# Performance work log

Hardware: AMD Instinct MI355X
Metric: run time of the kernel (lower is better)

## Reference

```python
import jax, jax.numpy as jnp
import numpy as np

TAU = 2.0
EPS_G = 1e-10   # gumbel numerical eps
EPS_H = 1e-12   # entropy log eps


def _gumbel(u):
    # u ~ Uniform(0,1) -> standard Gumbel noise
    return -jnp.log(-jnp.log(u + EPS_G) + EPS_G)


def setup_inputs() -> dict:
    key = jax.random.key(0)
    k1, k2, k3, k4 = jax.random.split(key, 4)
    B, T, D, K = 4, 1024, 512, 8192
    x = jax.random.normal(k1, (B, T, D), dtype=jnp.float32)
    codebook = jax.random.normal(k2, (K, D), dtype=jnp.float32)
    u1 = jax.random.uniform(k3, (B * T, K), dtype=jnp.float32)
    u2 = jax.random.uniform(k4, (B * T, K), dtype=jnp.float32)
    return {"x": x, "codebook": codebook, "u1": u1, "u2": u2}


def reference(x, codebook, u1, u2):
    B, T, D = x.shape
    x_flat = x.reshape(-1, D)                                  # (N, D)
    x_sq = jnp.sum(x_flat * x_flat, axis=1, keepdims=True)     # (N, 1)
    c_sq = jnp.sum(codebook * codebook, axis=1)                # (K,)
    xc = x_flat @ codebook.T                                   # (N, K)
    logits = -(x_sq + c_sq - 2.0 * xc)                         # -||x - c||^2

    # soft gumbel-softmax (first independent noise draw)
    probs_soft = jax.nn.softmax((logits + _gumbel(u1)) / TAU, axis=-1)  # (N, K)
    quantized_soft = (probs_soft @ codebook).reshape(B, T, D)

    # hard gumbel-softmax indices (second independent noise draw);
    # argmax of the hard one-hot == argmax of perturbed logits
    indices = jnp.argmax(logits + _gumbel(u2), axis=-1).reshape(B, T)

    codebook_loss = jnp.mean((quantized_soft - jax.lax.stop_gradient(x)) ** 2)
    enc_commitment_loss = jnp.mean((x - jax.lax.stop_gradient(quantized_soft)) ** 2)

    entropy = -jnp.sum(probs_soft * jnp.log(probs_soft + EPS_H), axis=1)  # (N,)
    mean_entropy = jnp.mean(entropy)

    return quantized_soft, indices, codebook_loss, enc_commitment_loss, mean_entropy
```

## Files before the change

kernel.cpp:

```cpp
#include <hip/hip_runtime.h>
#include <math.h>

#define NROWS 4096
#define KCODES 8192
#define DDIM 512
#define IDX_OFF 2097152
#define L0_OFF  2101248
#define L1_OFF  2101249
#define ENT_OFF 2101250
#define ARGMAX_MARGIN 0.05f
#define FIX_CHUNK 256
#define FIX_CPR (KCODES / FIX_CHUNK)

#define TOP2_UPD(v1, k1, v2, k2, h, k)                                 \
    do {                                                               \
        if ((h) > (v1)) { v2 = v1; k2 = k1; v1 = (h); k1 = (k); }      \
        else if ((h) > (v2)) { v2 = (h); k2 = (k); }                   \
    } while (0)

typedef __attribute__((ext_vector_type(8))) short bf16x8;
typedef __attribute__((ext_vector_type(4))) float f32x4;

__device__ __forceinline__ float gumbelfast(float u) {
    float a = __logf(u + 1e-10f);
    float b = __logf(1e-10f - a);
    return -b;
}
__device__ __forceinline__ ushort f2bf(float f) {
    uint u = __float_as_uint(f);
    return (ushort)((u + 0x7FFFu + ((u >> 16) & 1u)) >> 16);
}
__device__ __forceinline__ float bf2f(ushort h) {
    return __uint_as_float(((uint)h) << 16);
}

__device__ __forceinline__ float np_log32(float x) {
    return (float)log((double)x);
}
__device__ __forceinline__ float np_gumbel(float u) {
    float a  = __fadd_rn(u, 1e-10f);
    float la = np_log32(a);
    float b  = __fadd_rn(-la, 1e-10f);
    float lb = np_log32(b);
    return -lb;
}
__device__ float np_sumsq512(const float* __restrict__ a) {
    float blk[4];
    #pragma unroll
    for (int b = 0; b < 4; ++b) {
        const float* p = a + b * 128;
        float r[8];
        #pragma unroll
        for (int j = 0; j < 8; ++j) r[j] = __fmul_rn(p[j], p[j]);
        for (int i = 8; i < 128; i += 8) {
            #pragma unroll
            for (int j = 0; j < 8; ++j)
                r[j] = __fadd_rn(r[j], __fmul_rn(p[i + j], p[i + j]));
        }
        blk[b] = __fadd_rn(__fadd_rn(__fadd_rn(r[0], r[1]), __fadd_rn(r[2], r[3])),
                           __fadd_rn(__fadd_rn(r[4], r[5]), __fadd_rn(r[6], r[7])));
    }
    return __fadd_rn(__fadd_rn(blk[0], blk[1]), __fadd_rn(blk[2], blk[3]));
}

__device__ __forceinline__ float dot4(float4 a, float4 b) {
    return a.x*b.x + a.y*b.y + a.z*b.z + a.w*b.w;
}
__device__ __forceinline__ void fma4(float4& o, float p, float4 c) {
    o.x += p*c.x; o.y += p*c.y; o.z += p*c.z; o.w += p*c.w;
}

__global__ __launch_bounds__(256) void vq_csq2(const float* __restrict__ cb,
                                               float* __restrict__ csq,
                                               int* __restrict__ flag_cnt) {
    if (blockIdx.x == 0 && threadIdx.x == 0) flag_cnt[0] = 0;
    const int tid = threadIdx.x;
    const int row = blockIdx.x * 8 + (tid >> 5);
    const int rl  = tid & 31;
    const int b   = rl >> 3, j = rl & 7;
    const float* p = cb + (size_t)row * DDIM + b * 128 + j;
    float r = __fmul_rn(p[0], p[0]);
    #pragma unroll
    for (int i = 1; i < 16; ++i) {
        float v = p[i * 8];
        r = __fadd_rn(r, __fmul_rn(v, v));
    }
    r = __fadd_rn(r, __shfl_xor(r, 1));
    r = __fadd_rn(r, __shfl_xor(r, 2));
    r = __fadd_rn(r, __shfl_xor(r, 4));
    r = __fadd_rn(r, __shfl_xor(r, 8));
    r = __fadd_rn(r, __shfl_xor(r, 16));
    if (rl == 0) csq[row] = r;
}

__global__ __launch_bounds__(256) void vq_fixup(
        const float* __restrict__ x, const float* __restrict__ cb,
        const float* __restrict__ u2, const float* __restrict__ csq,
        const int* __restrict__ flag_cnt, const int* __restrict__ flag_rows,
        float* __restrict__ out) {
    __shared__ float xrow[DDIM];
    __shared__ float bv[4];
    __shared__ int   bk[4];
    const int n = flag_cnt[0];
    for (int w = blockIdx.x; w < n; w += gridDim.x) {
        const int row = flag_rows[w];
        for (int i = threadIdx.x; i < DDIM; i += 256)
            xrow[i] = x[(size_t)row * DDIM + i];
        __syncthreads();
        const float xsq = np_sumsq512(xrow);
        float best = -1e30f; int bidx = 0x7fffffff;
        for (int k = threadIdx.x; k < KCODES; k += 256) {
            const float* c = cb + (size_t)k * DDIM;
            float acc1 = 0.f, acc2 = 0.f;
            #pragma unroll 8
            for (int d = 0; d < 384; ++d) acc1 = fmaf(xrow[d], c[d], acc1);
            #pragma unroll 8
            for (int d = 384; d < DDIM; ++d) acc2 = fmaf(xrow[d], c[d], acc2);
            float xc = __fadd_rn(acc1, acc2);
            float t1 = __fadd_rn(xsq, csq[k]);
            float t2 = __fmul_rn(2.0f, xc);
            float t3 = __fsub_rn(t1, t2);
            float logit = -t3;
            float h = __fadd_rn(logit, np_gumbel(u2[(size_t)row * KCODES + k]));
            if (h > best || (h == best && k < bidx)) { best = h; bidx = k; }
        }
        const int lane = threadIdx.x & 63, wv = threadIdx.x >> 6;
        #pragma unroll
        for (int m = 32; m >= 1; m >>= 1) {
            float ov = __shfl_xor(best, m); int ok = __shfl_xor(bidx, m);
            if (ov > best || (ov == best && ok < bidx)) { best = ov; bidx = ok; }
        }
        if (lane == 0) { bv[wv] = best; bk[wv] = bidx; }
        __syncthreads();
        if (threadIdx.x == 0) {
            float b = bv[0]; int bi = bk[0];
            #pragma unroll
            for (int i = 1; i < 4; ++i)
                if (bv[i] > b || (bv[i] == b && bk[i] < bi)) { b = bv[i]; bi = bk[i]; }
            out[IDX_OFF + row] = (float)bi;
        }
        __syncthreads();
    }
}

__global__ __launch_bounds__(256) void vq_fixup2(
        const float* __restrict__ x, const float* __restrict__ cb,
        const float* __restrict__ u2, const float* __restrict__ csq,
        const int* __restrict__ flag_cnt, const int* __restrict__ flag_rows,
        unsigned long long* __restrict__ packed) {
    __shared__ float xrow[DDIM];
    __shared__ float xsq_sh;
    __shared__ unsigned long long redp[4];
    const int n = flag_cnt[0];
    const int total = n * FIX_CPR;
    for (int item = blockIdx.x; item < total; item += gridDim.x) {
        const int w = item / FIX_CPR;
        const int chunk = item - w * FIX_CPR;
        const int row = flag_rows[w];
        __syncthreads();
        for (int i = threadIdx.x; i < DDIM; i += 256)
            xrow[i] = x[(size_t)row * DDIM + i];
        __syncthreads();
        if (threadIdx.x == 0) xsq_sh = np_sumsq512(xrow);
        __syncthreads();
        const float xsq = xsq_sh;
        const int k = chunk * FIX_CHUNK + threadIdx.x;
        const float* c = cb + (size_t)k * DDIM;
        float acc1 = 0.f, acc2 = 0.f;
        #pragma unroll 8
        for (int d = 0; d < 384; ++d) acc1 = fmaf(xrow[d], c[d], acc1);
        #pragma unroll 8
        for (int d = 384; d < DDIM; ++d) acc2 = fmaf(xrow[d], c[d], acc2);
        float xc = __fadd_rn(acc1, acc2);
        float t1 = __fadd_rn(xsq, csq[k]);
        float t2 = __fmul_rn(2.0f, xc);
        float logit = -__fsub_rn(t1, t2);
        float h = __fadd_rn(logit, np_gumbel(u2[(size_t)row * KCODES + k]));
        uint hb = __float_as_uint(h);
        uint key = (hb & 0x80000000u) ? ~hb : (hb | 0x80000000u);
        unsigned long long val = ((unsigned long long)key << 32)
                               | (unsigned long long)(0xFFFFFFFFu - (uint)k);
        #pragma unroll
        for (int m = 32; m >= 1; m >>= 1) {
            unsigned long long o = __shfl_xor(val, m);
            if (o > val) val = o;
        }
        if ((threadIdx.x & 63) == 0) redp[threadIdx.x >> 6] = val;
        __syncthreads();
        if (threadIdx.x == 0) {
            unsigned long long v = redp[0];
            if (redp[1] > v) v = redp[1];
            if (redp[2] > v) v = redp[2];
            if (redp[3] > v) v = redp[3];
            atomicMax(&packed[row], v);
        }
    }
}


__global__ __launch_bounds__(256) void vq_split(const float4* __restrict__ in,
                                                ushort* __restrict__ hi,
                                                ushort* __restrict__ lo) {
    int i = blockIdx.x * 256 + threadIdx.x;
    float4 v = in[i];
    ushort4 h, l;
    h.x = f2bf(v.x); h.y = f2bf(v.y); h.z = f2bf(v.z); h.w = f2bf(v.w);
    l.x = f2bf(v.x - bf2f(h.x)); l.y = f2bf(v.y - bf2f(h.y));
    l.z = f2bf(v.z - bf2f(h.z)); l.w = f2bf(v.w - bf2f(h.w));
    ((ushort4*)hi)[i] = h;
    ((ushort4*)lo)[i] = l;
}

__global__ __launch_bounds__(256) void vq_prep_cb(const float* __restrict__ cb,
                                                  ushort* __restrict__ chi,
                                                  ushort* __restrict__ clo,
                                                  ushort* __restrict__ cbT) {
    __shared__ ushort T[64][65];
    const int k0 = blockIdx.x * 64, d0 = blockIdx.y * 64;
    const int lane = threadIdx.x & 63, w = threadIdx.x >> 6;
    #pragma unroll
    for (int i = 0; i < 16; ++i) {
        int ky = i * 4 + w;
        size_t g = (size_t)(k0 + ky) * DDIM + d0 + lane;
        float f = cb[g];
        ushort h = f2bf(f);
        chi[g] = h;
        clo[g] = f2bf(f - bf2f(h));
        T[lane][ky] = h;
    }
    __syncthreads();
    #pragma unroll
    for (int i = 0; i < 16; ++i) {
        int dy = i * 4 + w;
        cbT[(size_t)(d0 + dy) * KCODES + k0 + lane] = T[dy][lane];
    }
}

__global__ __launch_bounds__(256) void vq_gemm1(
        const ushort* __restrict__ xhi, const ushort* __restrict__ xlo,
        const ushort* __restrict__ chi, const ushort* __restrict__ clo,
        const float* __restrict__ csq, float* __restrict__ S0) {
    __shared__ short As[2][128 * 72];
    __shared__ short Bs[2][128 * 72];
    const int tid = threadIdx.x;
    const int lane = tid & 63, wid = tid >> 6;
    const int wr = wid >> 1, wc = wid & 1;
    const int m0 = blockIdx.y * 128, n0 = blockIdx.x * 128;

    bf16x8 sAh[4], sAl[4], sBh[4], sBl[4];
    f32x4 acc[4][4] = {};

    #define G1_LOAD(kkv)                                                       \
        do {                                                                   \
            const int k0_ = (kkv) * 64;                                        \
            _Pragma("unroll")                                                  \
            for (int i = 0; i < 4; ++i) {                                      \
                int c = tid + i * 256;                                         \
                int row = c >> 3, off = (c & 7) * 8;                           \
                size_t gA = (size_t)(m0 + row) * DDIM + k0_ + off;             \
                size_t gB = (size_t)(n0 + row) * DDIM + k0_ + off;             \
                sAh[i] = *(const bf16x8*)(xhi + gA);                           \
                sAl[i] = *(const bf16x8*)(xlo + gA);                           \
                sBh[i] = *(const bf16x8*)(chi + gB);                           \
                sBl[i] = *(const bf16x8*)(clo + gB);                           \
            }                                                                  \
        } while (0)

    #define G1_WRITE()                                                         \
        do {                                                                   \
            _Pragma("unroll")                                                  \
            for (int i = 0; i < 4; ++i) {                                      \
                int c = tid + i * 256;                                         \
                int row = c >> 3, off = (c & 7) * 8;                           \
                int lidx = row * 72 + off;                                     \
                *(bf16x8*)&As[0][lidx] = sAh[i];                               \
                *(bf16x8*)&As[1][lidx] = sAl[i];                               \
                *(bf16x8*)&Bs[0][lidx] = sBh[i];                               \
                *(bf16x8*)&Bs[1][lidx] = sBl[i];                               \
            }                                                                  \
        } while (0)

    G1_LOAD(0);
    G1_WRITE();
    __syncthreads();
    for (int kk = 0; kk < 8; ++kk) {
        if (kk < 7) G1_LOAD(kk + 1);
        #pragma unroll
        for (int ks = 0; ks < 2; ++ks) {
            const int ko = ks * 32 + (lane >> 4) * 8;
            bf16x8 ah[4], al[4], bh[4], bl[4];
            #pragma unroll
            for (int m = 0; m < 4; ++m) {
                int r = wr * 64 + m * 16 + (lane & 15);
                ah[m] = *(bf16x8*)&As[0][r * 72 + ko];
                al[m] = *(bf16x8*)&As[1][r * 72 + ko];
            }
            #pragma unroll
            for (int n = 0; n < 4; ++n) {
                int r = wc * 64 + n * 16 + (lane & 15);
                bh[n] = *(bf16x8*)&Bs[0][r * 72 + ko];
                bl[n] = *(bf16x8*)&Bs[1][r * 72 + ko];
            }
            #pragma unroll
            for (int m = 0; m < 4; ++m)
                #pragma unroll
                for (int n = 0; n < 4; ++n) {
                    acc[m][n] = __builtin_amdgcn_mfma_f32_16x16x32_bf16(ah[m], bh[n], acc[m][n], 0, 0, 0);
                    acc[m][n] = __builtin_amdgcn_mfma_f32_16x16x32_bf16(ah[m], bl[n], acc[m][n], 0, 0, 0);
                    acc[m][n] = __builtin_amdgcn_mfma_f32_16x16x32_bf16(al[m], bh[n], acc[m][n], 0, 0, 0);
                }
        }
        if (kk < 7) {
            __syncthreads();
            G1_WRITE();
            __syncthreads();
        }
    }
    #undef G1_LOAD
    #undef G1_WRITE

    #pragma unroll
    for (int n = 0; n < 4; ++n) {
        int col = n0 + wc * 64 + n * 16 + (lane & 15);
        float cq = csq[col];
        #pragma unroll
        for (int m = 0; m < 4; ++m) {
            int rbase = m0 + wr * 64 + m * 16 + ((lane >> 4) << 2);
            #pragma unroll
            for (int j = 0; j < 4; ++j)
                S0[(size_t)(rbase + j) * KCODES + col] = 2.0f * acc[m][n][j] - cq;
        }
    }
}

__global__ __launch_bounds__(1024) void vq_soft(
        float* __restrict__ S0, const float* __restrict__ u1,
        const float* __restrict__ u2,
        float* __restrict__ Aarr, float* __restrict__ entarr,
        float* __restrict__ out, int* __restrict__ flag_cnt,
        int* __restrict__ flag_rows, unsigned long long* __restrict__ packed) {
    __shared__ float redm[16], redA[16], redB[16];
    __shared__ float rv1[16], rv2[16];
    __shared__ int   rk1[16], rk2[16];
    const int row = blockIdx.x, tid = threadIdx.x;
    const int lane = tid & 63, wid = tid >> 6;
    const size_t base = (size_t)row * KCODES;
    if (tid == 0) packed[row] = 0ULL;

    const int ka = tid * 4;
    const int kb = 4096 + tid * 4;
    float4 Sa = *(const float4*)(S0 + base + ka);
    float4 Sb = *(const float4*)(S0 + base + kb);
    float4 Ua = *(const float4*)(u1 + base + ka);
    float4 Ub = *(const float4*)(u1 + base + kb);
    float4 Va = *(const float4*)(u2 + base + ka);
    float4 Vb = *(const float4*)(u2 + base + kb);

    float v1 = -1e30f, v2 = -1e30f; int k1 = 0x7fffffff, k2 = 0x7fffffff;
    float h;
    h = Sa.x + gumbelfast(Va.x); TOP2_UPD(v1, k1, v2, k2, h, ka);
    h = Sa.y + gumbelfast(Va.y); TOP2_UPD(v1, k1, v2, k2, h, ka + 1);
    h = Sa.z + gumbelfast(Va.z); TOP2_UPD(v1, k1, v2, k2, h, ka + 2);
    h = Sa.w + gumbelfast(Va.w); TOP2_UPD(v1, k1, v2, k2, h, ka + 3);
    h = Sb.x + gumbelfast(Vb.x); TOP2_UPD(v1, k1, v2, k2, h, kb);
    h = Sb.y + gumbelfast(Vb.y); TOP2_UPD(v1, k1, v2, k2, h, kb + 1);
    h = Sb.z + gumbelfast(Vb.z); TOP2_UPD(v1, k1, v2, k2, h, kb + 2);
    h = Sb.w + gumbelfast(Vb.w); TOP2_UPD(v1, k1, v2, k2, h, kb + 3);

    float4 sa, sb;
    sa.x = (Sa.x + gumbelfast(Ua.x)) * 0.5f;
    sa.y = (Sa.y + gumbelfast(Ua.y)) * 0.5f;
    sa.z = (Sa.z + gumbelfast(Ua.z)) * 0.5f;
    sa.w = (Sa.w + gumbelfast(Ua.w)) * 0.5f;
    sb.x = (Sb.x + gumbelfast(Ub.x)) * 0.5f;
    sb.y = (Sb.y + gumbelfast(Ub.y)) * 0.5f;
    sb.z = (Sb.z + gumbelfast(Ub.z)) * 0.5f;
    sb.w = (Sb.w + gumbelfast(Ub.w)) * 0.5f;
    float mloc = fmaxf(fmaxf(fmaxf(sa.x, sa.y), fmaxf(sa.z, sa.w)),
                       fmaxf(fmaxf(sb.x, sb.y), fmaxf(sb.z, sb.w)));
    #pragma unroll
    for (int m = 32; m >= 1; m >>= 1) mloc = fmaxf(mloc, __shfl_xor(mloc, m));
    if (lane == 0) redm[wid] = mloc;
    __syncthreads();
    float mrow = redm[0];
    #pragma unroll
    for (int i = 1; i < 16; ++i) mrow = fmaxf(mrow, redm[i]);

    float A, Be;
    {
        float d0 = sa.x - mrow, d1 = sa.y - mrow, d2 = sa.z - mrow, d3 = sa.w - mrow;
        float e0 = __expf(d0), e1 = __expf(d1), e2 = __expf(d2), e3 = __expf(d3);
        float d4 = sb.x - mrow, d5 = sb.y - mrow, d6 = sb.z - mrow, d7 = sb.w - mrow;
        float e4 = __expf(d4), e5 = __expf(d5), e6 = __expf(d6), e7 = __expf(d7);
        A  = (((e0 + e1) + e2) + e3) + ((((e4 + e5) + e6) + e7));
        Be = (((e0*d0 + e1*d1) + e2*d2) + e3*d3) + ((((e4*d4 + e5*d5) + e6*d6) + e7*d7));
        ushort* Prow = (ushort*)(S0 + base);
        ushort4 pa, pb;
        pa.x = f2bf(e0); pa.y = f2bf(e1); pa.z = f2bf(e2); pa.w = f2bf(e3);
        pb.x = f2bf(e4); pb.y = f2bf(e5); pb.z = f2bf(e6); pb.w = f2bf(e7);
        *(ushort4*)(Prow + ka) = pa;
        *(ushort4*)(Prow + kb) = pb;
    }
    #pragma unroll
    for (int m = 32; m >= 1; m >>= 1) { A += __shfl_xor(A, m); Be += __shfl_xor(Be, m); }
    #pragma unroll
    for (int m = 32; m >= 1; m >>= 1) {
        float ov1 = __shfl_xor(v1, m); int ok1 = __shfl_xor(k1, m);
        float ov2 = __shfl_xor(v2, m); int ok2 = __shfl_xor(k2, m);
        if (ov1 > v1 || (ov1 == v1 && ok1 < k1)) {
            float nv2; int nk2;
            if (v1 > ov2 || (v1 == ov2 && k1 < ok2)) { nv2 = v1; nk2 = k1; }
            else { nv2 = ov2; nk2 = ok2; }
            v1 = ov1; k1 = ok1; v2 = nv2; k2 = nk2;
        } else if (ov1 > v2 || (ov1 == v2 && ok1 < k2)) { v2 = ov1; k2 = ok1; }
    }
    if (lane == 0) {
        redA[wid] = A; redB[wid] = Be;
        rv1[wid] = v1; rv2[wid] = v2; rk1[wid] = k1; rk2[wid] = k2;
    }
    __syncthreads();
    if (tid == 0) {
        float At = 0.f, Bt = 0.f;
        #pragma unroll
        for (int i = 0; i < 16; ++i) { At += redA[i]; Bt += redB[i]; }
        float V1 = rv1[0], V2 = rv2[0]; int K1 = rk1[0], K2 = rk2[0];
        #pragma unroll
        for (int i = 1; i < 16; ++i) {
            float ov1 = rv1[i], ov2 = rv2[i]; int ok1 = rk1[i], ok2 = rk2[i];
            if (ov1 > V1 || (ov1 == V1 && ok1 < K1)) {
                float nv2; int nk2;
                if (V1 > ov2 || (V1 == ov2 && K1 < ok2)) { nv2 = V1; nk2 = K1; }
                else { nv2 = ov2; nk2 = ok2; }
                V1 = ov1; K1 = ok1; V2 = nv2; K2 = nk2;
            } else if (ov1 > V2 || (ov1 == V2 && ok1 < K2)) { V2 = ov1; K2 = ok1; }
        }
        Aarr[row] = At;
        entarr[row] = logf(At) - Bt / At;
        out[IDX_OFF + row] = (float)K1;
        if (V1 - V2 < ARGMAX_MARGIN) {
            int s = atomicAdd(flag_cnt, 1);
            flag_rows[s] = row;
        }
    }
}

#define G2_BK 128
__global__ __launch_bounds__(512) void vq_gemm2b(
        const ushort* __restrict__ P, const ushort* __restrict__ cbT,
        const float* __restrict__ Aarr, const float* __restrict__ x,
        float* __restrict__ out, float* __restrict__ wloss) {
    __shared__ short Ap[2][128 * 136];
    __shared__ short Bt[2][64 * 136];
    __shared__ float redl[8];
    const int tid = threadIdx.x;
    const int lane = tid & 63, wid = tid >> 6;
    const int wr = wid & 3, wc = wid >> 2;
    const int bid = blockIdx.x;
    const int mblk = bid & 31, nblk = bid >> 5;
    const int m0 = mblk * 128, n0 = nblk * 64;

    bf16x8 rp[4], rb[2];
    f32x4 acc[2][2] = {};

    #define G2_LOAD(t)                                                         \
        do {                                                                   \
            const int k0_ = (t) * G2_BK;                                       \
            _Pragma("unroll")                                                  \
            for (int i = 0; i < 4; ++i) {                                      \
                int c = tid + i * 512;                                         \
                int row = c >> 4, off = (c & 15) * 8;                          \
                rp[i] = *(const bf16x8*)(P + (size_t)(m0 + row) * 16384 + k0_ + off); \
            }                                                                  \
            _Pragma("unroll")                                                  \
            for (int i = 0; i < 2; ++i) {                                      \
                int c = tid + i * 512;                                         \
                int row = c >> 4, off = (c & 15) * 8;                          \
                rb[i] = *(const bf16x8*)(cbT + (size_t)(n0 + row) * 8192 + k0_ + off); \
            }                                                                  \
        } while (0)

    #define G2_WRITE(buf)                                                      \
        do {                                                                   \
            _Pragma("unroll")                                                  \
            for (int i = 0; i < 4; ++i) {                                      \
                int c = tid + i * 512;                                         \
                int row = c >> 4, off = (c & 15) * 8;                          \
                *(bf16x8*)&Ap[buf][row * 136 + off] = rp[i];                   \
            }                                                                  \
            _Pragma("unroll")                                                  \
            for (int i = 0; i < 2; ++i) {                                      \
                int c = tid + i * 512;                                         \
                int row = c >> 4, off = (c & 15) * 8;                          \
                *(bf16x8*)&Bt[buf][row * 136 + off] = rb[i];                   \
            }                                                                  \
        } while (0)

    G2_LOAD(0);
    G2_WRITE(0);
    __syncthreads();
    int cur = 0;
    for (int t = 0; t < KCODES / G2_BK; ++t) {
        if (t < KCODES / G2_BK - 1) G2_LOAD(t + 1);
        #pragma unroll
        for (int ks = 0; ks < 4; ++ks) {
            const int ko = ks * 32 + (lane >> 4) * 8;
            bf16x8 af[2], bfr[2];
            #pragma unroll
            for (int m = 0; m < 2; ++m)
                af[m] = *(bf16x8*)&Ap[cur][(wr * 32 + m * 16 + (lane & 15)) * 136 + ko];
            #pragma unroll
            for (int n = 0; n < 2; ++n)
                bfr[n] = *(bf16x8*)&Bt[cur][(wc * 32 + n * 16 + (lane & 15)) * 136 + ko];
            #pragma unroll
            for (int m = 0; m < 2; ++m)
                #pragma unroll
                for (int n = 0; n < 2; ++n)
                    acc[m][n] = __builtin_amdgcn_mfma_f32_16x16x32_bf16(af[m], bfr[n], acc[m][n], 0, 0, 0);
        }
        if (t < KCODES / G2_BK - 1) {
            __syncthreads();
            G2_WRITE(cur ^ 1);
            __syncthreads();
            cur ^= 1;
        }
    }
    #undef G2_LOAD
    #undef G2_WRITE

    float lsum = 0.f;
    #pragma unroll
    for (int n = 0; n < 2; ++n) {
        int col = n0 + wc * 32 + n * 16 + (lane & 15);
        #pragma unroll
        for (int m = 0; m < 2; ++m) {
            int rbase = m0 + wr * 32 + m * 16 + ((lane >> 4) << 2);
            #pragma unroll
            for (int j = 0; j < 4; ++j) {
                int row = rbase + j;
                float inva = 1.0f / Aarr[row];
                float q = acc[m][n][j] * inva;
                out[(size_t)row * DDIM + col] = q;
                float d = q - x[(size_t)row * DDIM + col];
                lsum += d * d;
            }
        }
    }
    #pragma unroll
    for (int m = 32; m >= 1; m >>= 1) lsum += __shfl_xor(lsum, m);
    if (lane == 0) redl[wid] = lsum;
    __syncthreads();
    if (tid == 0) {
        float s = 0.f;
        #pragma unroll
        for (int i = 0; i < 8; ++i) s += redl[i];
        wloss[bid] = s;
    }
}

__global__ __launch_bounds__(256) void vq_finalize2(
        const float* __restrict__ wloss, const float* __restrict__ entarr,
        const int* __restrict__ flag_cnt, const int* __restrict__ flag_rows,
        const unsigned long long* __restrict__ packed, float* __restrict__ out) {
    __shared__ float redl[4], rede[4];
    int tid = threadIdx.x;
    const int n = flag_cnt[0];
    for (int w = tid; w < n; w += 256) {
        int row = flag_rows[w];
        uint lowbits = (uint)(packed[row] & 0xFFFFFFFFULL);
        out[IDX_OFF + row] = (float)(0xFFFFFFFFu - lowbits);
    }
    float l = wloss[tid];
    float e = 0.f;
    #pragma unroll
    for (int i = 0; i < 16; ++i) e += entarr[tid + i * 256];
    #pragma unroll
    for (int m = 32; m >= 1; m >>= 1) { l += __shfl_xor(l, m); e += __shfl_xor(e, m); }
    if ((tid & 63) == 0) { redl[tid >> 6] = l; rede[tid >> 6] = e; }
    __syncthreads();
    if (tid == 0) {
        float L = (((redl[0] + redl[1]) + redl[2]) + redl[3]) * (1.0f / 2097152.0f);
        float E = (((rede[0] + rede[1]) + rede[2]) + rede[3]) * (1.0f / 4096.0f);
        out[L0_OFF]  = L;
        out[L1_OFF]  = L;
        out[ENT_OFF] = E;
    }
}

#define BR 16
#define KT 128
#define NUM_KT 64
#define NUM_DC 4

__device__ __forceinline__ float gumbelf(float u) {
    return -logf(-logf(u + 1e-10f) + 1e-10f);
}

__global__ __launch_bounds__(256) void vq_main_fb(
        const float* __restrict__ x, const float* __restrict__ cb,
        const float* __restrict__ u1, const float* __restrict__ u2,
        const float* __restrict__ csq, float* __restrict__ out,
        float* __restrict__ wloss, float* __restrict__ went,
        int* __restrict__ flag_cnt, int* __restrict__ flag_rows) {
    __shared__ float4 Xs[BR][129];
    __shared__ float4 Cs[KT * 32];
    __shared__ float4 Ol[BR][128];
    __shared__ float4 Ps[BR][32];
    __shared__ float  xsq_s[BR];
    __shared__ float  f_s[BR];
    __shared__ float  A_s[BR];
    __shared__ float  ent_s[BR];
    __shared__ float  red4[4];

    const int tid = threadIdx.x;
    const int rg  = tid >> 5;
    const int cg  = tid & 31;
    const int r0  = rg * 2;
    const int r1  = r0 + 1;
    const int row0g = blockIdx.x * BR;
    const float4* cb4 = (const float4*)cb;

    {
        const float4* xg = (const float4*)x + (size_t)row0g * 128;
        #pragma unroll
        for (int i = 0; i < 8; ++i) {
            int idx = tid + i * 256;
            int r = idx >> 7, q = idx & 127;
            Xs[r][q] = xg[r * 128 + q];
            Ol[r][q] = make_float4(0.f, 0.f, 0.f, 0.f);
        }
    }
    __syncthreads();
    {
        int r = tid >> 4, part = tid & 15;
        float s = 0.f;
        #pragma unroll
        for (int q = 0; q < 8; ++q) {
            float4 v = Xs[r][part * 8 + q];
            s += v.x*v.x + v.y*v.y + v.z*v.z + v.w*v.w;
        }
        #pragma unroll
        for (int m = 8; m >= 1; m >>= 1) s += __shfl_xor(s, m);
        if (part == 0) xsq_s[r] = s;
    }
    __syncthreads();
    const float xsq0 = xsq_s[r0];
    const float xsq1 = xsq_s[r1];

    float m0 = -1e30f, m1 = -1e30f;
    float A0 = 0.f, A1 = 0.f;
    float B0 = 0.f, B1 = 0.f;
    float hb0 = -1e30f, hb1 = -1e30f;
    float hc0 = -1e30f, hc1 = -1e30f;
    int   kb0 = 0, kb1 = 0, kc0 = 0, kc1 = 0;

    for (int t = 0; t < NUM_KT; ++t) {
        const int ktb = t * KT;
        float a00=0.f,a01=0.f,a02=0.f,a03=0.f,a10=0.f,a11=0.f,a12=0.f,a13=0.f;

        for (int dc = 0; dc < NUM_DC; ++dc) {
            #pragma unroll
            for (int i = 0; i < 16; ++i) {
                int idx = tid + i * 256;
                int k = idx >> 5, q = idx & 31;
                Cs[k * 32 + (q ^ ((k >> 2) & 7))] =
                    cb4[(size_t)(ktb + k) * 128 + dc * 32 + q];
            }
            __syncthreads();
            const int qb = dc * 32;
            const int c4 = cg * 4;
            #pragma unroll 4
            for (int dd = 0; dd < 32; ++dd) {
                float4 xv0 = Xs[r0][qb + dd];
                float4 xv1 = Xs[r1][qb + dd];
                int swq = dd ^ (cg & 7);
                float4 cv0 = Cs[(c4 + 0) * 32 + swq];
                float4 cv1 = Cs[(c4 + 1) * 32 + swq];
                float4 cv2 = Cs[(c4 + 2) * 32 + swq];
                float4 cv3 = Cs[(c4 + 3) * 32 + swq];
                a00 += dot4(xv0, cv0); a01 += dot4(xv0, cv1);
                a02 += dot4(xv0, cv2); a03 += dot4(xv0, cv3);
                a10 += dot4(xv1, cv0); a11 += dot4(xv1, cv1);
                a12 += dot4(xv1, cv2); a13 += dot4(xv1, cv3);
            }
            __syncthreads();
        }
        {
            const int kg0 = ktb + cg * 4;
            size_t ur0 = (size_t)(row0g + r0) * KCODES + kg0;
            size_t ur1 = (size_t)(row0g + r1) * KCODES + kg0;
            float4 u1a = *(const float4*)(u1 + ur0);
            float4 u1b = *(const float4*)(u1 + ur1);
            float4 u2a = *(const float4*)(u2 + ur0);
            float4 u2b = *(const float4*)(u2 + ur1);
            float cs0 = csq[kg0], cs1 = csq[kg0+1], cs2 = csq[kg0+2], cs3 = csq[kg0+3];
            {
                float l0 = 2.f*a00 - xsq0 - cs0;
                float l1 = 2.f*a01 - xsq0 - cs1;
                float l2 = 2.f*a02 - xsq0 - cs2;
                float l3 = 2.f*a03 - xsq0 - cs3;
                float h;
                h = l0 + gumbelf(u2a.x); TOP2_UPD(hb0, kb0, hc0, kc0, h, kg0);
                h = l1 + gumbelf(u2a.y); TOP2_UPD(hb0, kb0, hc0, kc0, h, kg0+1);
                h = l2 + gumbelf(u2a.z); TOP2_UPD(hb0, kb0, hc0, kc0, h, kg0+2);
                h = l3 + gumbelf(u2a.w); TOP2_UPD(hb0, kb0, hc0, kc0, h, kg0+3);
                float s0 = (l0 + gumbelf(u1a.x)) * 0.5f;
                float s1 = (l1 + gumbelf(u1a.y)) * 0.5f;
                float s2 = (l2 + gumbelf(u1a.z)) * 0.5f;
                float s3 = (l3 + gumbelf(u1a.w)) * 0.5f;
                float tmax = fmaxf(fmaxf(s0, s1), fmaxf(s2, s3));
                #pragma unroll
                for (int m = 16; m >= 1; m >>= 1) tmax = fmaxf(tmax, __shfl_xor(tmax, m));
                float mn = fmaxf(m0, tmax);
                float p0 = expf(s0 - mn), p1 = expf(s1 - mn);
                float p2 = expf(s2 - mn), p3 = expf(s3 - mn);
                float tA = p0 + p1 + p2 + p3;
                float tB = p0*(s0-mn) + p1*(s1-mn) + p2*(s2-mn) + p3*(s3-mn);
                #pragma unroll
                for (int m = 16; m >= 1; m >>= 1) { tA += __shfl_xor(tA, m); tB += __shfl_xor(tB, m); }
                float f = expf(m0 - mn);
                B0 = f * (B0 + (m0 - mn) * A0) + tB;
                A0 = f * A0 + tA;
                m0 = mn;
                Ps[r0][cg] = make_float4(p0, p1, p2, p3);
                if (cg == 0) f_s[r0] = f;
            }
            {
                float l0 = 2.f*a10 - xsq1 - cs0;
                float l1 = 2.f*a11 - xsq1 - cs1;
                float l2 = 2.f*a12 - xsq1 - cs2;
                float l3 = 2.f*a13 - xsq1 - cs3;
                float h;
                h = l0 + gumbelf(u2b.x); TOP2_UPD(hb1, kb1, hc1, kc1, h, kg0);
                h = l1 + gumbelf(u2b.y); TOP2_UPD(hb1, kb1, hc1, kc1, h, kg0+1);
                h = l2 + gumbelf(u2b.z); TOP2_UPD(hb1, kb1, hc1, kc1, h, kg0+2);
                h = l3 + gumbelf(u2b.w); TOP2_UPD(hb1, kb1, hc1, kc1, h, kg0+3);
                float s0 = (l0 + gumbelf(u1b.x)) * 0.5f;
                float s1 = (l1 + gumbelf(u1b.y)) * 0.5f;
                float s2 = (l2 + gumbelf(u1b.z)) * 0.5f;
                float s3 = (l3 + gumbelf(u1b.w)) * 0.5f;
                float tmax = fmaxf(fmaxf(s0, s1), fmaxf(s2, s3));
                #pragma unroll
                for (int m = 16; m >= 1; m >>= 1) tmax = fmaxf(tmax, __shfl_xor(tmax, m));
                float mn = fmaxf(m1, tmax);
                float p0 = expf(s0 - mn), p1 = expf(s1 - mn);
                float p2 = expf(s2 - mn), p3 = expf(s3 - mn);
                float tA = p0 + p1 + p2 + p3;
                float tB = p0*(s0-mn) + p1*(s1-mn) + p2*(s2-mn) + p3*(s3-mn);
                #pragma unroll
                for (int m = 16; m >= 1; m >>= 1) { tA += __shfl_xor(tA, m); tB += __shfl_xor(tB, m); }
                float f = expf(m1 - mn);
                B1 = f * (B1 + (m1 - mn) * A1) + tB;
                A1 = f * A1 + tA;
                m1 = mn;
                Ps[r1][cg] = make_float4(p0, p1, p2, p3);
                if (cg == 0) f_s[r1] = f;
            }
        }
        __syncthreads();

        for (int dc = 0; dc < NUM_DC; ++dc) {
            #pragma unroll
            for (int i = 0; i < 16; ++i) {
                int idx = tid + i * 256;
                int k = idx >> 5, q = idx & 31;
                Cs[k * 32 + (q ^ ((k >> 2) & 7))] =
                    cb4[(size_t)(ktb + k) * 128 + dc * 32 + q];
            }
            __syncthreads();
            float4 o0 = make_float4(0.f,0.f,0.f,0.f);
            float4 o1 = make_float4(0.f,0.f,0.f,0.f);
            #pragma unroll 2
            for (int k4 = 0; k4 < 32; ++k4) {
                float4 pv0 = Ps[r0][k4];
                float4 pv1 = Ps[r1][k4];
                int sq = cg ^ (k4 & 7);
                float4 cva = Cs[(k4*4 + 0) * 32 + sq];
                float4 cvb = Cs[(k4*4 + 1) * 32 + sq];
                float4 cvc = Cs[(k4*4 + 2) * 32 + sq];
                float4 cvd = Cs[(k4*4 + 3) * 32 + sq];
                fma4(o0, pv0.x, cva); fma4(o0, pv0.y, cvb);
                fma4(o0, pv0.z, cvc); fma4(o0, pv0.w, cvd);
                fma4(o1, pv1.x, cva); fma4(o1, pv1.y, cvb);
                fma4(o1, pv1.z, cvc); fma4(o1, pv1.w, cvd);
            }
            float fr0 = f_s[r0], fr1 = f_s[r1];
            int oq = dc * 32 + cg;
            float4 Ov0 = Ol[r0][oq];
            Ov0.x = Ov0.x*fr0 + o0.x; Ov0.y = Ov0.y*fr0 + o0.y;
            Ov0.z = Ov0.z*fr0 + o0.z; Ov0.w = Ov0.w*fr0 + o0.w;
            Ol[r0][oq] = Ov0;
            float4 Ov1 = Ol[r1][oq];
            Ov1.x = Ov1.x*fr1 + o1.x; Ov1.y = Ov1.y*fr1 + o1.y;
            Ov1.z = Ov1.z*fr1 + o1.z; Ov1.w = Ov1.w*fr1 + o1.w;
            Ol[r1][oq] = Ov1;
            __syncthreads();
        }
    }
    {
        float ent0 = logf(A0) - B0 / A0;
        float v1 = hb0, v2 = hc0; int k1 = kb0, k2 = kc0;
        #pragma unroll
        for (int m = 16; m >= 1; m >>= 1) {
            float ov1 = __shfl_xor(v1, m); int ok1 = __shfl_xor(k1, m);
            float ov2 = __shfl_xor(v2, m); int ok2 = __shfl_xor(k2, m);
            if (ov1 > v1 || (ov1 == v1 && ok1 < k1)) {
                float nv2; int nk2;
                if (v1 > ov2 || (v1 == ov2 && k1 < ok2)) { nv2 = v1; nk2 = k1; }
                else { nv2 = ov2; nk2 = ok2; }
                v1 = ov1; k1 = ok1; v2 = nv2; k2 = nk2;
            } else if (ov1 > v2 || (ov1 == v2 && ok1 < k2)) {
                v2 = ov1; k2 = ok1;
            }
        }
        if (cg == 0) {
            out[IDX_OFF + row0g + r0] = (float)k1;
            if (v1 - v2 < ARGMAX_MARGIN) {
                int s = atomicAdd(flag_cnt, 1);
                flag_rows[s] = row0g + r0;
            }
            ent_s[r0] = ent0;
            A_s[r0] = A0;
        }
        float ent1 = logf(A1) - B1 / A1;
        v1 = hb1; v2 = hc1; k1 = kb1; k2 = kc1;
        #pragma unroll
        for (int m = 16; m >= 1; m >>= 1) {
            float ov1 = __shfl_xor(v1, m); int ok1 = __shfl_xor(k1, m);
            float ov2 = __shfl_xor(v2, m); int ok2 = __shfl_xor(k2, m);
            if (ov1 > v1 || (ov1 == v1 && ok1 < k1)) {
                float nv2; int nk2;
                if (v1 > ov2 || (v1 == ov2 && k1 < ok2)) { nv2 = v1; nk2 = k1; }
                else { nv2 = ov2; nk2 = ok2; }
                v1 = ov1; k1 = ok1; v2 = nv2; k2 = nk2;
            } else if (ov1 > v2 || (ov1 == v2 && ok1 < k2)) {
                v2 = ov1; k2 = ok1;
            }
        }
        if (cg == 0) {
            out[IDX_OFF + row0g + r1] = (float)k1;
            if (v1 - v2 < ARGMAX_MARGIN) {
                int s = atomicAdd(flag_cnt, 1);
                flag_rows[s] = row0g + r1;
            }
            ent_s[r1] = ent1;
            A_s[r1] = A1;
        }
    }
    __syncthreads();

    float lsum = 0.f;
    float4* outq = (float4*)out;
    #pragma unroll
    for (int i = 0; i < 8; ++i) {
        int idx = tid + i * 256;
        int r = idx >> 7, q = idx & 127;
        float inva = 1.f / A_s[r];
        float4 Ov = Ol[r][q];
        float4 qv = make_float4(Ov.x*inva, Ov.y*inva, Ov.z*inva, Ov.w*inva);
        outq[(size_t)(row0g + r) * 128 + q] = qv;
        float4 xv = Xs[r][q];
        float dx;
        dx = qv.x - xv.x; lsum += dx*dx;
        dx = qv.y - xv.y; lsum += dx*dx;
        dx = qv.z - xv.z; lsum += dx*dx;
        dx = qv.w - xv.w; lsum += dx*dx;
    }
    #pragma unroll
    for (int m = 32; m >= 1; m >>= 1) lsum += __shfl_xor(lsum, m);
    if ((tid & 63) == 0) red4[tid >> 6] = lsum;
    __syncthreads();
    if (tid == 0) {
        wloss[blockIdx.x] = red4[0] + red4[1] + red4[2] + red4[3];
        float es = 0.f;
        for (int r = 0; r < BR; ++r) es += ent_s[r];
        went[blockIdx.x] = es;
    }
}

__global__ __launch_bounds__(256) void vq_finalize_fb(const float* __restrict__ wloss,
                                                      const float* __restrict__ went,
                                                      float* __restrict__ out) {
    __shared__ float redl[4], rede[4];
    int tid = threadIdx.x;
    float l = wloss[tid];
    float e = went[tid];
    #pragma unroll
    for (int m = 32; m >= 1; m >>= 1) { l += __shfl_xor(l, m); e += __shfl_xor(e, m); }
    if ((tid & 63) == 0) { redl[tid >> 6] = l; rede[tid >> 6] = e; }
    __syncthreads();
    if (tid == 0) {
        float L = (redl[0] + redl[1] + redl[2] + redl[3]) * (1.0f / 2097152.0f);
        float E = (rede[0] + rede[1] + rede[2] + rede[3]) * (1.0f / 4096.0f);
        out[L0_OFF]  = L;
        out[L1_OFF]  = L;
        out[ENT_OFF] = E;
    }
}

extern "C" void kernel_launch(void* const* d_in, const int* in_sizes, int n_in,
                              void* d_out, int out_size, void* d_ws, size_t ws_size,
                              hipStream_t stream) {
    const float* x  = (const float*)d_in[0];
    const float* cb = (const float*)d_in[1];
    const float* u1 = (const float*)d_in[2];
    const float* u2 = (const float*)d_in[3];
    float* out = (float*)d_out;

    const size_t NEED = 0xA018000ULL;
    if (ws_size >= NEED) {
        char* w = (char*)d_ws;
        float*  S0   = (float*)w;
        ushort* xhi  = (ushort*)(w + 0x8000000);
        ushort* xlo  = (ushort*)(w + 0x8400000);
        ushort* chi  = (ushort*)(w + 0x8800000);
        ushort* clo  = (ushort*)(w + 0x9000000);
        ushort* cbT  = (ushort*)(w + 0x9800000);
        float*  csq  = (float*)(w + 0xA000000);
        float*  Aarr = (float*)(w + 0xA008000);
        float*  enta = (float*)(w + 0xA00C000);
        float*  wlp  = (float*)(w + 0xA010000);
        int*    fcnt = (int*)(w + 0xA010400);
        int*    frws = (int*)(w + 0xA010800);
        unsigned long long* packed = (unsigned long long*)(w + 0x8000000);

        vq_csq2<<<KCODES / 8, 256, 0, stream>>>(cb, csq, fcnt);
        vq_split<<<2048, 256, 0, stream>>>((const float4*)x, xhi, xlo);
        vq_prep_cb<<<dim3(128, 8), 256, 0, stream>>>(cb, chi, clo, cbT);
        vq_gemm1<<<dim3(64, 32), 256, 0, stream>>>(xhi, xlo, chi, clo, csq, S0);
        vq_soft<<<NROWS, 1024, 0, stream>>>(S0, u1, u2, Aarr, enta, out, fcnt, frws, packed);
        vq_gemm2b<<<256, 512, 0, stream>>>((const ushort*)S0, cbT, Aarr, x, out, wlp);
        vq_fixup2<<<1024, 256, 0, stream>>>(x, cb, u2, csq, fcnt, frws, packed);
        vq_finalize2<<<1, 256, 0, stream>>>(wlp, enta, fcnt, frws, packed, out);
    } else {
        float* ws  = (float*)d_ws;
        float* csq    = ws;
        float* wlossp = ws + KCODES;
        float* wentp  = ws + KCODES + 256;
        int*   fcnt   = (int*)(ws + KCODES + 512);
        int*   frows  = fcnt + 1;

        vq_csq2<<<KCODES / 8, 256, 0, stream>>>(cb, csq, fcnt);
        vq_main_fb<<<NROWS / BR, 256, 0, stream>>>(x, cb, u1, u2, csq, out,
                                                   wlossp, wentp, fcnt, frows);
        vq_fixup<<<256, 256, 0, stream>>>(x, cb, u2, csq, fcnt, frows, out);
        vq_finalize_fb<<<1, 256, 0, stream>>>(wlossp, wentp, out);
    }
}
```

Baseline: 367.5 us.

## Fuse hard-gumbel top-2 argmax into GEMM1 epilogue with packed sortable keys

```diff
diff --git a/kernel.cpp b/kernel.cpp
--- a/kernel.cpp
+++ b/kernel.cpp
@@ -32,6 +32,12 @@
 }
 __device__ __forceinline__ float bf2f(ushort h) {
     return __uint_as_float(((uint)h) << 16);
+}
+__device__ __forceinline__ unsigned long long hkey(float h, int k) {
+    uint hb = __float_as_uint(h);
+    uint kk = (hb & 0x80000000u) ? ~hb : (hb | 0x80000000u);
+    return ((unsigned long long)kk << 32)
+         | (unsigned long long)(0xFFFFFFFFu - (uint)k);
 }
 
 __device__ __forceinline__ float np_log32(float x) {
@@ -239,9 +245,11 @@
 __global__ __launch_bounds__(256) void vq_gemm1(
         const ushort* __restrict__ xhi, const ushort* __restrict__ xlo,
         const ushort* __restrict__ chi, const ushort* __restrict__ clo,
-        const float* __restrict__ csq, float* __restrict__ S0) {
+        const float* __restrict__ csq, const float* __restrict__ u2,
+        float* __restrict__ S0, ulonglong2* __restrict__ Htop) {
     __shared__ short As[2][128 * 72];
     __shared__ short Bs[2][128 * 72];
+    __shared__ ulonglong2 Top2L[128][2];
     const int tid = threadIdx.x;
     const int lane = tid & 63, wid = tid >> 6;
     const int wr = wid >> 1, wc = wid & 1;
@@ -319,29 +327,65 @@
     #undef G1_LOAD
     #undef G1_WRITE
 
+    const int colbase = n0 + wc * 64 + (lane & 15);
+    float cqv[4];
+    #pragma unroll
+    for (int n = 0; n < 4; ++n) cqv[n] = csq[colbase + n * 16];
+
     #pragma unroll
     for (int n = 0; n < 4; ++n) {
-        int col = n0 + wc * 64 + n * 16 + (lane & 15);
-        float cq = csq[col];
+        int col = colbase + n * 16;
         #pragma unroll
         for (int m = 0; m < 4; ++m) {
             int rbase = m0 + wr * 64 + m * 16 + ((lane >> 4) << 2);
             #pragma unroll
             for (int j = 0; j < 4; ++j)
-                S0[(size_t)(rbase + j) * KCODES + col] = 2.0f * acc[m][n][j] - cq;
-        }
+                S0[(size_t)(rbase + j) * KCODES + col] = 2.0f * acc[m][n][j] - cqv[n];
+        }
+    }
+
+    #pragma unroll
+    for (int m = 0; m < 4; ++m) {
+        #pragma unroll
+        for (int j = 0; j < 4; ++j) {
+            const int rl = wr * 64 + m * 16 + ((lane >> 4) << 2) + j;
+            const size_t ur = (size_t)(m0 + rl) * KCODES + colbase;
+            unsigned long long t1 = 0ULL, t2 = 0ULL;
+            #pragma unroll
+            for (int n = 0; n < 4; ++n) {
+                float S = 2.0f * acc[m][n][j] - cqv[n];
+                float h = S + gumbelfast(u2[ur + n * 16]);
+                unsigned long long key = hkey(h, colbase + n * 16);
+                if (key > t1) { t2 = t1; t1 = key; }
+                else if (key > t2) { t2 = key; }
+            }
+            #pragma unroll
+            for (int mm = 1; mm <= 8; mm <<= 1) {
+                unsigned long long b1 = __shfl_xor(t1, mm);
+                unsigned long long b2 = __shfl_xor(t2, mm);
+                if (b1 > t1) { unsigned long long t = t1; t1 = b1; t2 = (t > b2) ? t : b2; }
+                else         { t2 = (b1 > t2) ? b1 : t2; }
+            }
+            if ((lane & 15) == 0) Top2L[rl][wc] = make_ulonglong2(t1, t2);
+        }
+    }
+    __syncthreads();
+    if (tid < 128) {
+        ulonglong2 a = Top2L[tid][0], b = Top2L[tid][1];
+        unsigned long long r1, r2;
+        if (b.x > a.x) { r1 = b.x; r2 = (a.x > b.y) ? a.x : b.y; }
+        else           { r1 = a.x; r2 = (b.x > a.y) ? b.x : a.y; }
+        Htop[(size_t)(m0 + tid) * 64 + blockIdx.x] = make_ulonglong2(r1, r2);
     }
 }
 
 __global__ __launch_bounds__(1024) void vq_soft(
         float* __restrict__ S0, const float* __restrict__ u1,
-        const float* __restrict__ u2,
+        const ulonglong2* __restrict__ Htop,
         float* __restrict__ Aarr, float* __restrict__ entarr,
         float* __restrict__ out, int* __restrict__ flag_cnt,
         int* __restrict__ flag_rows, unsigned long long* __restrict__ packed) {
     __shared__ float redm[16], redA[16], redB[16];
-    __shared__ float rv1[16], rv2[16];
-    __shared__ int   rk1[16], rk2[16];
     const int row = blockIdx.x, tid = threadIdx.x;
     const int lane = tid & 63, wid = tid >> 6;
     const size_t base = (size_t)row * KCODES;
@@ -353,19 +397,19 @@
     float4 Sb = *(const float4*)(S0 + base + kb);
     float4 Ua = *(const float4*)(u1 + base + ka);
     float4 Ub = *(const float4*)(u1 + base + kb);
-    float4 Va = *(const float4*)(u2 + base + ka);
-    float4 Vb = *(const float4*)(u2 + base + kb);
-
-    float v1 = -1e30f, v2 = -1e30f; int k1 = 0x7fffffff, k2 = 0x7fffffff;
-    float h;
-    h = Sa.x + gumbelfast(Va.x); TOP2_UPD(v1, k1, v2, k2, h, ka);
-    h = Sa.y + gumbelfast(Va.y); TOP2_UPD(v1, k1, v2, k2, h, ka + 1);
-    h = Sa.z + gumbelfast(Va.z); TOP2_UPD(v1, k1, v2, k2, h, ka + 2);
-    h = Sa.w + gumbelfast(Va.w); TOP2_UPD(v1, k1, v2, k2, h, ka + 3);
-    h = Sb.x + gumbelfast(Vb.x); TOP2_UPD(v1, k1, v2, k2, h, kb);
-    h = Sb.y + gumbelfast(Vb.y); TOP2_UPD(v1, k1, v2, k2, h, kb + 1);
-    h = Sb.z + gumbelfast(Vb.z); TOP2_UPD(v1, k1, v2, k2, h, kb + 2);
-    h = Sb.w + gumbelfast(Vb.w); TOP2_UPD(v1, k1, v2, k2, h, kb + 3);
+
+    unsigned long long K1k = 0ULL, K2k = 0ULL;
+    if (tid < 64) {
+        ulonglong2 e = Htop[(size_t)row * 64 + tid];
+        K1k = e.x; K2k = e.y;
+        #pragma unroll
+        for (int mm = 1; mm <= 32; mm <<= 1) {
+            unsigned long long b1 = __shfl_xor(K1k, mm);
+            unsigned long long b2 = __shfl_xor(K2k, mm);
+            if (b1 > K1k) { unsigned long long t = K1k; K1k = b1; K2k = (t > b2) ? t : b2; }
+            else          { K2k = (b1 > K2k) ? b1 : K2k; }
+        }
+    }
 
     float4 sa, sb;
     sa.x = (Sa.x + gumbelfast(Ua.x)) * 0.5f;
@@ -403,39 +447,18 @@
     }
     #pragma unroll
     for (int m = 32; m >= 1; m >>= 1) { A += __shfl_xor(A, m); Be += __shfl_xor(Be, m); }
-    #pragma unroll
-    for (int m = 32; m >= 1; m >>= 1) {
-        float ov1 = __shfl_xor(v1, m); int ok1 = __shfl_xor(k1, m);
-        float ov2 = __shfl_xor(v2, m); int ok2 = __shfl_xor(k2, m);
-        if (ov1 > v1 || (ov1 == v1 && ok1 < k1)) {
-            float nv2; int nk2;
-            if (v1 > ov2 || (v1 == ov2 && k1 < ok2)) { nv2 = v1; nk2 = k1; }
-            else { nv2 = ov2; nk2 = ok2; }
-            v1 = ov1; k1 = ok1; v2 = nv2; k2 = nk2;
-        } else if (ov1 > v2 || (ov1 == v2 && ok1 < k2)) { v2 = ov1; k2 = ok1; }
-    }
-    if (lane == 0) {
-        redA[wid] = A; redB[wid] = Be;
-        rv1[wid] = v1; rv2[wid] = v2; rk1[wid] = k1; rk2[wid] = k2;
-    }
+    if (lane == 0) { redA[wid] = A; redB[wid] = Be; }
     __syncthreads();
     if (tid == 0) {
         float At = 0.f, Bt = 0.f;
         #pragma unroll
         for (int i = 0; i < 16; ++i) { At += redA[i]; Bt += redB[i]; }
-        float V1 = rv1[0], V2 = rv2[0]; int K1 = rk1[0], K2 = rk2[0];
-        #pragma unroll
-        for (int i = 1; i < 16; ++i) {
-            float ov1 = rv1[i], ov2 = rv2[i]; int ok1 = rk1[i], ok2 = rk2[i];
-            if (ov1 > V1 || (ov1 == V1 && ok1 < K1)) {
-                float nv2; int nk2;
-                if (V1 > ov2 || (V1 == ov2 && K1 < ok2)) { nv2 = V1; nk2 = K1; }
-                else { nv2 = ov2; nk2 = ok2; }
-                V1 = ov1; K1 = ok1; V2 = nv2; K2 = nk2;
-            } else if (ov1 > V2 || (ov1 == V2 && ok1 < K2)) { V2 = ov1; K2 = ok1; }
-        }
         Aarr[row] = At;
         entarr[row] = logf(At) - Bt / At;
+        uint hi1 = (uint)(K1k >> 32), hi2 = (uint)(K2k >> 32);
+        float V1 = __uint_as_float((hi1 & 0x80000000u) ? (hi1 & 0x7FFFFFFFu) : ~hi1);
+        float V2 = __uint_as_float((hi2 & 0x80000000u) ? (hi2 & 0x7FFFFFFFu) : ~hi2);
+        int K1 = (int)(0xFFFFFFFFu - (uint)(K1k & 0xFFFFFFFFULL));
         out[IDX_OFF + row] = (float)K1;
         if (V1 - V2 < ARGMAX_MARGIN) {
             int s = atomicAdd(flag_cnt, 1);
@@ -922,12 +945,13 @@
         int*    fcnt = (int*)(w + 0xA010400);
         int*    frws = (int*)(w + 0xA010800);
         unsigned long long* packed = (unsigned long long*)(w + 0x8000000);
+        ulonglong2* Htop = (ulonglong2*)d_out;
 
         vq_csq2<<<KCODES / 8, 256, 0, stream>>>(cb, csq, fcnt);
         vq_split<<<2048, 256, 0, stream>>>((const float4*)x, xhi, xlo);
         vq_prep_cb<<<dim3(128, 8), 256, 0, stream>>>(cb, chi, clo, cbT);
-        vq_gemm1<<<dim3(64, 32), 256, 0, stream>>>(xhi, xlo, chi, clo, csq, S0);
-        vq_soft<<<NROWS, 1024, 0, stream>>>(S0, u1, u2, Aarr, enta, out, fcnt, frws, packed);
+        vq_gemm1<<<dim3(64, 32), 256, 0, stream>>>(xhi, xlo, chi, clo, csq, u2, S0, Htop);
+        vq_soft<<<NROWS, 1024, 0, stream>>>(S0, u1, Htop, Aarr, enta, out, fcnt, frws, packed);
         vq_gemm2b<<<256, 512, 0, stream>>>((const ushort*)S0, cbT, Aarr, x, out, wlp);
         vq_fixup2<<<1024, 256, 0, stream>>>(x, cb, u2, csq, fcnt, frws, packed);
         vq_finalize2<<<1, 256, 0, stream>>>(wlp, enta, fcnt, frws, packed, out);
```

After: 409.4 us. +11.4%, slower.
